# Performance work log

Measured on AMD Instinct MI355X. Metric: run time of the kernel, lower is better.

The kernel has to match this reference:

```python
import jax, jax.numpy as jnp
import numpy as np

B, T, C, HS = 4, 2048, 1024, 64

def setup_inputs() -> dict:
    key = jax.random.key(0)
    k1, k2, k3, k4 = jax.random.split(key, 4)
    # weights stored as [n_embd, head_size] so projection is x @ W
    scale = C ** -0.5
    return {
        "x": jax.random.normal(k1, (B, T, C), dtype=jnp.float32),
        "Wq": jax.random.normal(k2, (C, HS), dtype=jnp.float32) * scale,
        "Wk": jax.random.normal(k3, (C, HS), dtype=jnp.float32) * scale,
        "Wv": jax.random.normal(k4, (C, HS), dtype=jnp.float32) * scale,
    }

def reference(x, Wq, Wk, Wv):
    # single-head causal attention: softmax(QK^T / sqrt(hs)) V, dropout p=0 (eval)
    q = x @ Wq  # [B,T,hs]
    k = x @ Wk
    v = x @ Wv
    hs = k.shape[-1]
    wei = jnp.einsum('bqh,bkh->bqk', q, k) * (hs ** -0.5)  # [B,T,T]
    causal = jnp.tril(jnp.ones((q.shape[1], q.shape[1]), dtype=bool))
    wei = jnp.where(causal[None, :, :], wei, -jnp.inf)
    wei = jax.nn.softmax(wei, axis=-1)
    out = jnp.einsum('bqk,bkh->bqh', wei, v)  # [B,T,hs]
    return out
```

## Files before the change

kernel.cpp:

```cpp
#include <hip/hip_runtime.h>
#include <stdint.h>

#define NB 4
#define NT 2048
#define NC 1024
#define NH 64
#define NM (NB*NT)

typedef unsigned short u16;
typedef unsigned int u32;
typedef __bf16 bf16_t;
typedef float f32x4 __attribute__((ext_vector_type(4)));
typedef bf16_t bf16x8 __attribute__((ext_vector_type(8)));
typedef u16 u16x8 __attribute__((ext_vector_type(8)));
typedef u16 u16x4 __attribute__((ext_vector_type(4)));

__device__ __forceinline__ u16 f2b(float f) {
  return __builtin_bit_cast(u16, (bf16_t)f);
}
__device__ __forceinline__ float b2f(u16 u) {
  return (float)__builtin_bit_cast(bf16_t, u);
}

__device__ __forceinline__ void gl16(const void* g, void* l) {
  __builtin_amdgcn_global_load_lds(
      (const __attribute__((address_space(1))) u32*)g,
      (__attribute__((address_space(3))) u32*)l, 16, 0, 0);
}

__global__ __launch_bounds__(256) void wt_kernel(const float* __restrict__ Wq,
                                                 const float* __restrict__ Wk,
                                                 const float* __restrict__ Wv,
                                                 u16* __restrict__ wt) {
  __shared__ float t[64][65];
  const int m = blockIdx.x >> 4;
  const int kt = blockIdx.x & 15;
  const int k0 = kt * 64;
  const float* W = (m == 0) ? Wq : (m == 1) ? Wk : Wv;
  {
    const int r = threadIdx.x >> 2, c4 = threadIdx.x & 3;
    #pragma unroll
    for (int j = 0; j < 4; ++j) {
      const float4 f = *(const float4*)(W + (size_t)(k0 + r) * NH + c4 * 16 + j * 4);
      t[r][c4 * 16 + j * 4 + 0] = f.x;
      t[r][c4 * 16 + j * 4 + 1] = f.y;
      t[r][c4 * 16 + j * 4 + 2] = f.z;
      t[r][c4 * 16 + j * 4 + 3] = f.w;
    }
  }
  __syncthreads();
  const int n = threadIdx.x >> 2, kc = threadIdx.x & 3;
  u16x8 a, b;
  #pragma unroll
  for (int j = 0; j < 8; ++j) a[j] = f2b(t[kc * 16 + j][n]);
  #pragma unroll
  for (int j = 0; j < 8; ++j) b[j] = f2b(t[kc * 16 + 8 + j][n]);
  u16* dst = wt + ((size_t)(m * 64 + n)) * NC + k0 + kc * 16;
  *(u16x8*)dst = a;
  *(u16x8*)(dst + 8) = b;
}

__global__ __launch_bounds__(256) void proj_kernel(const float* __restrict__ x,
                                                   const u16* __restrict__ wt,
                                                   u16* __restrict__ pc) {
  __shared__ float sA[64 * 128];
  __shared__ u16 sB[192 * 128];
  const int tid = threadIdx.x;
  const int lane = tid & 63;
  const int cg = tid >> 6;
  const int g = lane >> 4;
  const int li = lane & 15;
  const int msel = blockIdx.x >> 2;
  const int split = blockIdx.x & 3;
  const int row0 = msel * 64;
  const int wbase = tid & 0xC0;

  const f32x4 zero = {0.f, 0.f, 0.f, 0.f};
  f32x4 acc[4][3];
  #pragma unroll
  for (int rt = 0; rt < 4; ++rt)
    #pragma unroll
    for (int f = 0; f < 3; ++f) acc[rt][f] = zero;

  auto stage = [&](int h) {
    const int kf = split * 256 + h * 128;
    #pragma unroll
    for (int j = 0; j < 8; ++j) {
      const int slot = j * 256 + tid;
      const int r = slot >> 5, c = slot & 31;
      gl16(x + (size_t)(row0 + r) * NC + kf + ((c ^ (r & 7)) * 4),
           (char*)sA + (j * 256 + wbase) * 16);
    }
    #pragma unroll
    for (int j = 0; j < 12; ++j) {
      const int slot = j * 256 + tid;
      const int n = slot >> 4, c = slot & 15;
      gl16(wt + (size_t)n * NC + kf + ((c ^ (n & 7)) * 8),
           (char*)sB + (j * 256 + wbase) * 16);
    }
  };

  #pragma unroll
  for (int h = 0; h < 2; ++h) {
    stage(h);
    asm volatile("s_waitcnt vmcnt(0)" ::: "memory");
    __syncthreads();
    #pragma unroll
    for (int s = 0; s < 4; ++s) {
      bf16x8 aF[4];
      #pragma unroll
      for (int rt = 0; rt < 4; ++rt) {
        const int r = rt * 16 + li;
        const int c0 = s * 8 + g * 2;
        const f32x4 a0 = *(const f32x4*)&sA[r * 128 + ((c0 ^ (r & 7)) * 4)];
        const f32x4 a1 = *(const f32x4*)&sA[r * 128 + (((c0 + 1) ^ (r & 7)) * 4)];
        bf16x8 v;
        v[0]=(bf16_t)a0.x; v[1]=(bf16_t)a0.y; v[2]=(bf16_t)a0.z; v[3]=(bf16_t)a0.w;
        v[4]=(bf16_t)a1.x; v[5]=(bf16_t)a1.y; v[6]=(bf16_t)a1.z; v[7]=(bf16_t)a1.w;
        aF[rt] = v;
      }
      #pragma unroll
      for (int f = 0; f < 3; ++f) {
        const int n = (cg * 3 + f) * 16 + li;
        const bf16x8 bF = *(const bf16x8*)&sB[n * 128 + (((s * 4 + g) ^ (n & 7)) * 8)];
        #pragma unroll
        for (int rt = 0; rt < 4; ++rt)
          acc[rt][f] = __builtin_amdgcn_mfma_f32_16x16x32_bf16(aF[rt], bF, acc[rt][f], 0, 0, 0);
      }
    }
    if (h == 0) __syncthreads();
  }

  #pragma unroll
  for (int rt = 0; rt < 4; ++rt) {
    const int rr0 = row0 + rt * 16 + g * 4;
    #pragma unroll
    for (int f = 0; f < 3; ++f) {
      const int col = (cg * 3 + f) * 16 + li;
      #pragma unroll
      for (int i = 0; i < 4; ++i)
        pc[((size_t)split * NM + rr0 + i) * 192 + col] = f2b(acc[rt][f][i]);
    }
  }
}

__global__ __launch_bounds__(256) void pmerge_kernel(const u16* __restrict__ pc,
                                                     u16* __restrict__ qo,
                                                     u16* __restrict__ ko,
                                                     u16* __restrict__ vto) {
  const int gid = blockIdx.x * 256 + threadIdx.x;
  const int row = gid / 48;
  const int c0 = (gid % 48) * 4;
  float s0 = 0.f, s1 = 0.f, s2 = 0.f, s3 = 0.f;
  #pragma unroll
  for (int s = 0; s < 4; ++s) {
    const u16x4 v = *(const u16x4*)&pc[((size_t)s * NM + row) * 192 + c0];
    s0 += b2f(v[0]); s1 += b2f(v[1]); s2 += b2f(v[2]); s3 += b2f(v[3]);
  }
  u16x4 o;
  o[0] = f2b(s0); o[1] = f2b(s1); o[2] = f2b(s2); o[3] = f2b(s3);
  if (c0 < 64) {
    *(u16x4*)&qo[(size_t)row * NH + c0] = o;
  } else if (c0 < 128) {
    *(u16x4*)&ko[(size_t)row * NH + (c0 - 64)] = o;
  } else {
    const int hs0 = c0 - 128;
    const int bidx = row >> 11;
    const int tt = row & 2047;
    const int tile = tt >> 6, off = tt & 63;
    #pragma unroll
    for (int i = 0; i < 4; ++i)
      vto[(((size_t)(bidx * 32 + tile) * 64) + hs0 + i) * 64 + off] = o[i];
  }
}

struct AttnGrp {
  union {
    u16 K[2][32 * 64];
    struct { float mo[2][16][64]; float ml[2][16]; } mg;
  } u;
};

__global__ __launch_bounds__(512) void attn_kernel(const u16* __restrict__ qg,
                                                   const u16* __restrict__ kg,
                                                   const u16* __restrict__ vtg,
                                                   float* __restrict__ out) {
  __shared__ AttnGrp grp[8];
  __shared__ u16 sP[8][16 * 32];
  const int tid = threadIdx.x;
  const int lane = tid & 63;
  const int s = tid >> 6;
  const int g = lane >> 4;
  const int li = lane & 15;
  const int jA = blockIdx.x & 63;
  const int bb = blockIdx.x >> 6;
  const int jB = 127 - jA;
  const size_t bt0 = (size_t)bb * NT;
  const int q0A = jA * 16, q0B = jB * 16;
  const int n1 = (jA >> 1) + 1;
  const int nB = 64 - (jA >> 1);

  bf16x8 aqA[2], aqB[2];
  #pragma unroll
  for (int ks = 0; ks < 2; ++ks) {
    aqA[ks] = *(const bf16x8*)(qg + (bt0 + q0A + li) * NH + ks * 32 + g * 8);
    aqB[ks] = *(const bf16x8*)(qg + (bt0 + q0B + li) * NH + ks * 32 + g * 8);
  }

  const f32x4 zero = {0.f, 0.f, 0.f, 0.f};
  f32x4 oA[4], oB[4];
  float lA[4], lB[4];
  #pragma unroll
  for (int i = 0; i < 4; ++i) { oA[i] = zero; oB[i] = zero; lA[i] = 0.f; lB[i] = 0.f; }

  auto stageK = [&](int t, int b) {
    const size_t kbase = bt0 + (size_t)t * 32;
    #pragma unroll
    for (int jj = 0; jj < 4; ++jj) {
      const int idx = jj * 64 + lane;
      const int n = idx >> 3, c = idx & 7;
      gl16(kg + (kbase + n) * NH + ((c ^ (n & 7)) * 8),
           (char*)grp[s].u.K[b] + jj * 1024);
    }
  };

  auto computeT = [&](const bf16x8 (&aq)[2], f32x4 (&o)[4], float (&ls)[4],
                      int q0, int kv0, int b, const bf16x8 (&vf)[4]) {
    f32x4 sc2[2] = {zero, zero};
    #pragma unroll
    for (int ks = 0; ks < 2; ++ks) {
      #pragma unroll
      for (int fn = 0; fn < 2; ++fn) {
        const int n = fn * 16 + li;
        const bf16x8 bk = *(const bf16x8*)&grp[s].u.K[b][n * 64 + (((ks * 4 + g) ^ (n & 7)) * 8)];
        sc2[fn] = __builtin_amdgcn_mfma_f32_16x16x32_bf16(aq[ks], bk, sc2[fn], 0, 0, 0);
      }
    }
    const bool needmask = (kv0 + 31 > q0);
    #pragma unroll
    for (int fn = 0; fn < 2; ++fn) {
      #pragma unroll
      for (int i = 0; i < 4; ++i) {
        const int q = g * 4 + i;
        float v = sc2[fn][i] * 0.125f;
        if (needmask && (kv0 + fn * 16 + li > q0 + q)) v = -1e30f;
        const float e = __expf(v);
        ls[i] += e;
        const int kc = fn * 2 + (li >> 3);
        sP[s][q * 32 + ((kc ^ (q & 3) ^ ((q >> 2) & 3)) * 8) + (li & 7)] = f2b(e);
      }
    }
    const bf16x8 pa = *(const bf16x8*)&sP[s][li * 32 + ((g ^ (li & 3) ^ ((li >> 2) & 3)) * 8)];
    #pragma unroll
    for (int fn = 0; fn < 4; ++fn)
      o[fn] = __builtin_amdgcn_mfma_f32_16x16x32_bf16(pa, vf[fn], o[fn], 0, 0, 0);
  };

  stageK(s, 0);
  int k = 0;
  for (int t = s; t < nB; t += 8, ++k) {
    bf16x8 vf[4];
    const size_t vrow = ((size_t)(bb * 32 + (t >> 1))) * 64;
    const int hoff = (t & 1) * 32;
    #pragma unroll
    for (int fn = 0; fn < 4; ++fn)
      vf[fn] = *(const bf16x8*)(vtg + (vrow + fn * 16 + li) * 64 + hoff + g * 8);

    if (t + 8 < nB) {
      stageK(t + 8, (k + 1) & 1);
      asm volatile("s_waitcnt vmcnt(8)" ::: "memory");
    } else {
      asm volatile("s_waitcnt vmcnt(4)" ::: "memory");
    }
    const int b = k & 1;
    computeT(aqB, oB, lB, q0B, t * 32, b, vf);
    if (t < n1) computeT(aqA, oA, lA, q0A, t * 32, b, vf);
  }

  #pragma unroll
  for (int i = 0; i < 4; ++i) {
    float a = lA[i], c = lB[i];
    a += __shfl_xor(a, 1); c += __shfl_xor(c, 1);
    a += __shfl_xor(a, 2); c += __shfl_xor(c, 2);
    a += __shfl_xor(a, 4); c += __shfl_xor(c, 4);
    a += __shfl_xor(a, 8); c += __shfl_xor(c, 8);
    lA[i] = a; lB[i] = c;
  }

  #pragma unroll
  for (int fn = 0; fn < 4; ++fn) {
    #pragma unroll
    for (int i = 0; i < 4; ++i) {
      grp[s].u.mg.mo[0][g * 4 + i][fn * 16 + li] = oA[fn][i];
      grp[s].u.mg.mo[1][g * 4 + i][fn * 16 + li] = oB[fn][i];
    }
  }
  if (li == 0) {
    #pragma unroll
    for (int i = 0; i < 4; ++i) {
      grp[s].u.mg.ml[0][g * 4 + i] = lA[i];
      grp[s].u.mg.ml[1][g * 4 + i] = lB[i];
    }
  }
  __syncthreads();

  {
    const int base = tid * 4;
    const int tile = base >> 10;
    const int r = (base >> 6) & 15;
    const int c0 = base & 63;
    float L = 0.f;
    f32x4 acc = zero;
    #pragma unroll
    for (int s8 = 0; s8 < 8; ++s8) {
      L += grp[s8].u.mg.ml[tile][r];
      acc += *(const f32x4*)&grp[s8].u.mg.mo[tile][r][c0];
    }
    const int row = (tile ? q0B : q0A) + r;
    const float inv = 1.f / L;
    acc *= inv;
    *(f32x4*)&out[(bt0 + row) * NH + c0] = acc;
  }
}

extern "C" void kernel_launch(void* const* d_in, const int* in_sizes, int n_in,
                              void* d_out, int out_size, void* d_ws, size_t ws_size,
                              hipStream_t stream) {
  (void)in_sizes; (void)n_in; (void)out_size; (void)ws_size;
  const float* x  = (const float*)d_in[0];
  const float* Wq = (const float*)d_in[1];
  const float* Wk = (const float*)d_in[2];
  const float* Wv = (const float*)d_in[3];
  float* out = (float*)d_out;
  char* ws = (char*)d_ws;
  u16* qb  = (u16*)(ws);
  u16* kb  = (u16*)(ws + (1u << 20));
  u16* vtb = (u16*)(ws + (2u << 20));
  u16* wtb = (u16*)(ws + (3u << 20));
  u16* pcb = (u16*)(ws + (3u << 20) + (512u << 10));
  hipLaunchKernelGGL(wt_kernel,     dim3(48),   dim3(256), 0, stream, Wq, Wk, Wv, wtb);
  hipLaunchKernelGGL(proj_kernel,   dim3(512),  dim3(256), 0, stream, x, wtb, pcb);
  hipLaunchKernelGGL(pmerge_kernel, dim3(1536), dim3(256), 0, stream, pcb, qb, kb, vtb);
  hipLaunchKernelGGL(attn_kernel,   dim3(256),  dim3(512), 0, stream, qb, kb, vtb, out);
}
```

Measured before the change: 44.12 us.

## Keep the weight slice resident in LDS and stream double-buffered x tiles in projection

The projection kernel now loads its K-slice of the transposed weights into LDS once. It then loops over eight 16-row tiles of x (128 rows per block), double-buffering the x tiles so the next load overlaps compute, and writes partial results after each tile. When the workspace is large enough it splits K eight ways instead of four, and the merge kernel sums eight partial buffers. This cuts repeated weight loading and LDS footprint, but doubles the partial-sum traffic through global memory and adds a barrier per tile with fewer MFMAs per wave between barriers.

```diff
diff --git a/kernel.cpp b/kernel.cpp
--- a/kernel.cpp
+++ b/kernel.cpp
@@ -60,90 +60,87 @@
   *(u16x8*)(dst + 8) = b;
 }
 
+template<int KLEN>
 __global__ __launch_bounds__(256) void proj_kernel(const float* __restrict__ x,
                                                    const u16* __restrict__ wt,
                                                    u16* __restrict__ pc) {
-  __shared__ float sA[64 * 128];
-  __shared__ u16 sB[192 * 128];
+  constexpr int BCH = KLEN / 8;
+  constexpr int ACH = KLEN / 4;
+  constexpr int NBJ = 192 * BCH / 256;
+  constexpr int NAJ = (16 * ACH) / 256;
+  __shared__ u16 sB[192 * KLEN];
+  __shared__ float sA[2][16 * KLEN];
   const int tid = threadIdx.x;
   const int lane = tid & 63;
   const int cg = tid >> 6;
   const int g = lane >> 4;
   const int li = lane & 15;
-  const int msel = blockIdx.x >> 2;
-  const int split = blockIdx.x & 3;
-  const int row0 = msel * 64;
+  const int row0 = blockIdx.x * 128;
+  const int split = blockIdx.y;
+  const int kbase = split * KLEN;
   const int wbase = tid & 0xC0;
 
   const f32x4 zero = {0.f, 0.f, 0.f, 0.f};
-  f32x4 acc[4][3];
-  #pragma unroll
-  for (int rt = 0; rt < 4; ++rt)
-    #pragma unroll
-    for (int f = 0; f < 3; ++f) acc[rt][f] = zero;
-
-  auto stage = [&](int h) {
-    const int kf = split * 256 + h * 128;
-    #pragma unroll
-    for (int j = 0; j < 8; ++j) {
+
+  auto stageB = [&]() {
+    #pragma unroll
+    for (int j = 0; j < NBJ; ++j) {
       const int slot = j * 256 + tid;
-      const int r = slot >> 5, c = slot & 31;
-      gl16(x + (size_t)(row0 + r) * NC + kf + ((c ^ (r & 7)) * 4),
-           (char*)sA + (j * 256 + wbase) * 16);
-    }
-    #pragma unroll
-    for (int j = 0; j < 12; ++j) {
+      const int n = slot / BCH, c = slot % BCH;
+      gl16(wt + (size_t)n * NC + kbase + ((c ^ (n & 7)) * 8),
+           (char*)sB + (j * 256 + wbase) * 16);
+    }
+  };
+  auto stageA = [&](int t, int buf) {
+    const int r0 = row0 + t * 16;
+    #pragma unroll
+    for (int j = 0; j < NAJ; ++j) {
       const int slot = j * 256 + tid;
-      const int n = slot >> 4, c = slot & 15;
-      gl16(wt + (size_t)n * NC + kf + ((c ^ (n & 7)) * 8),
-           (char*)sB + (j * 256 + wbase) * 16);
+      const int r = slot / ACH, c = slot % ACH;
+      gl16(x + (size_t)(r0 + r) * NC + kbase + ((c ^ (r & 7)) * 4),
+           (char*)sA[buf] + (j * 256 + wbase) * 16);
     }
   };
 
-  #pragma unroll
-  for (int h = 0; h < 2; ++h) {
-    stage(h);
-    asm volatile("s_waitcnt vmcnt(0)" ::: "memory");
-    __syncthreads();
-    #pragma unroll
-    for (int s = 0; s < 4; ++s) {
-      bf16x8 aF[4];
-      #pragma unroll
-      for (int rt = 0; rt < 4; ++rt) {
-        const int r = rt * 16 + li;
-        const int c0 = s * 8 + g * 2;
-        const f32x4 a0 = *(const f32x4*)&sA[r * 128 + ((c0 ^ (r & 7)) * 4)];
-        const f32x4 a1 = *(const f32x4*)&sA[r * 128 + (((c0 + 1) ^ (r & 7)) * 4)];
-        bf16x8 v;
-        v[0]=(bf16_t)a0.x; v[1]=(bf16_t)a0.y; v[2]=(bf16_t)a0.z; v[3]=(bf16_t)a0.w;
-        v[4]=(bf16_t)a1.x; v[5]=(bf16_t)a1.y; v[6]=(bf16_t)a1.z; v[7]=(bf16_t)a1.w;
-        aF[rt] = v;
-      }
+  stageB();
+  stageA(0, 0);
+  __syncthreads();
+
+  for (int t = 0; t < 8; ++t) {
+    const int cur = t & 1;
+    if (t < 7) stageA(t + 1, cur ^ 1);
+    f32x4 acc[3];
+    #pragma unroll
+    for (int f = 0; f < 3; ++f) acc[f] = zero;
+    #pragma unroll
+    for (int s = 0; s < KLEN / 32; ++s) {
+      const int r = li;
+      const int c0 = s * 8 + g * 2;
+      const f32x4 a0 = *(const f32x4*)&sA[cur][r * KLEN + ((c0 ^ (r & 7)) * 4)];
+      const f32x4 a1 = *(const f32x4*)&sA[cur][r * KLEN + (((c0 + 1) ^ (r & 7)) * 4)];
+      bf16x8 a;
+      a[0]=(bf16_t)a0.x; a[1]=(bf16_t)a0.y; a[2]=(bf16_t)a0.z; a[3]=(bf16_t)a0.w;
+      a[4]=(bf16_t)a1.x; a[5]=(bf16_t)a1.y; a[6]=(bf16_t)a1.z; a[7]=(bf16_t)a1.w;
       #pragma unroll
       for (int f = 0; f < 3; ++f) {
         const int n = (cg * 3 + f) * 16 + li;
-        const bf16x8 bF = *(const bf16x8*)&sB[n * 128 + (((s * 4 + g) ^ (n & 7)) * 8)];
-        #pragma unroll
-        for (int rt = 0; rt < 4; ++rt)
-          acc[rt][f] = __builtin_amdgcn_mfma_f32_16x16x32_bf16(aF[rt], bF, acc[rt][f], 0, 0, 0);
+        const bf16x8 bF = *(const bf16x8*)&sB[n * KLEN + (((s * 4 + g) ^ (n & 7)) * 8)];
+        acc[f] = __builtin_amdgcn_mfma_f32_16x16x32_bf16(a, bF, acc[f], 0, 0, 0);
       }
     }
-    if (h == 0) __syncthreads();
-  }
-
-  #pragma unroll
-  for (int rt = 0; rt < 4; ++rt) {
-    const int rr0 = row0 + rt * 16 + g * 4;
+    const int rr0 = row0 + t * 16 + g * 4;
     #pragma unroll
     for (int f = 0; f < 3; ++f) {
       const int col = (cg * 3 + f) * 16 + li;
       #pragma unroll
       for (int i = 0; i < 4; ++i)
-        pc[((size_t)split * NM + rr0 + i) * 192 + col] = f2b(acc[rt][f][i]);
-    }
-  }
-}
-
+        pc[((size_t)split * NM + rr0 + i) * 192 + col] = f2b(acc[f][i]);
+    }
+    __syncthreads();
+  }
+}
+
+template<int KSPL>
 __global__ __launch_bounds__(256) void pmerge_kernel(const u16* __restrict__ pc,
                                                      u16* __restrict__ qo,
                                                      u16* __restrict__ ko,
@@ -153,7 +150,7 @@
   const int c0 = (gid % 48) * 4;
   float s0 = 0.f, s1 = 0.f, s2 = 0.f, s3 = 0.f;
   #pragma unroll
-  for (int s = 0; s < 4; ++s) {
+  for (int s = 0; s < KSPL; ++s) {
     const u16x4 v = *(const u16x4*)&pc[((size_t)s * NM + row) * 192 + c0];
     s0 += b2f(v[0]); s1 += b2f(v[1]); s2 += b2f(v[2]); s3 += b2f(v[3]);
   }
@@ -326,7 +323,7 @@
 extern "C" void kernel_launch(void* const* d_in, const int* in_sizes, int n_in,
                               void* d_out, int out_size, void* d_ws, size_t ws_size,
                               hipStream_t stream) {
-  (void)in_sizes; (void)n_in; (void)out_size; (void)ws_size;
+  (void)in_sizes; (void)n_in; (void)out_size;
   const float* x  = (const float*)d_in[0];
   const float* Wq = (const float*)d_in[1];
   const float* Wk = (const float*)d_in[2];
@@ -338,8 +335,15 @@
   u16* vtb = (u16*)(ws + (2u << 20));
   u16* wtb = (u16*)(ws + (3u << 20));
   u16* pcb = (u16*)(ws + (3u << 20) + (512u << 10));
-  hipLaunchKernelGGL(wt_kernel,     dim3(48),   dim3(256), 0, stream, Wq, Wk, Wv, wtb);
-  hipLaunchKernelGGL(proj_kernel,   dim3(512),  dim3(256), 0, stream, x, wtb, pcb);
-  hipLaunchKernelGGL(pmerge_kernel, dim3(1536), dim3(256), 0, stream, pcb, qb, kb, vtb);
-  hipLaunchKernelGGL(attn_kernel,   dim3(256),  dim3(512), 0, stream, qb, kb, vtb, out);
-}
+
+  hipLaunchKernelGGL(wt_kernel, dim3(48), dim3(256), 0, stream, Wq, Wk, Wv, wtb);
+  const size_t need8 = (3u << 20) + (512u << 10) + (size_t)8 * NM * 192 * 2;
+  if (ws_size >= need8) {
+    hipLaunchKernelGGL((proj_kernel<128>),  dim3(64, 8), dim3(256), 0, stream, x, wtb, pcb);
+    hipLaunchKernelGGL((pmerge_kernel<8>),  dim3(1536),  dim3(256), 0, stream, pcb, qb, kb, vtb);
+  } else {
+    hipLaunchKernelGGL((proj_kernel<256>),  dim3(64, 4), dim3(256), 0, stream, x, wtb, pcb);
+    hipLaunchKernelGGL((pmerge_kernel<4>),  dim3(1536),  dim3(256), 0, stream, pcb, qb, kb, vtb);
+  }
+  hipLaunchKernelGGL(attn_kernel, dim3(256), dim3(512), 0, stream, qb, kb, vtb, out);
+}
```

New measurement: 43.41 us. About the same (-1.6%).
